# Optimization experiments

Measured on AMD Instinct MI355X. Metric: run time of the kernel, lower is better.

Reference implementation:

```python
import jax, jax.numpy as jnp
import numpy as np


def setup_inputs() -> dict:
    key = jax.random.key(0)
    kq, kk, kv, kl = jax.random.split(key, 4)
    B, Nq, Nk, D, Dv = 16, 2048, 2048, 128, 128
    queries = jax.random.normal(kq, (B, Nq, D), dtype=jnp.float32)
    keys = jax.random.normal(kk, (B, Nk, D), dtype=jnp.float32)
    values = jax.random.normal(kv, (B, Nk, Dv), dtype=jnp.float32)
    valid_lens = jax.random.randint(kl, (B,), 0, 2048, dtype=jnp.int64)
    return {"queries": queries, "keys": keys, "values": values, "valid_lens": valid_lens}


def reference(queries, keys, values, valid_lens):
    # queries: (B, Nq, d), keys: (B, Nk, d), values: (B, Nk, dv), valid_lens: (B,)
    d = queries.shape[-1]
    scores = jnp.einsum('bqd,bkd->bqk', queries, keys) / jnp.sqrt(jnp.asarray(d, queries.dtype))
    # masked_softmax: original sets masked score positions to 1e-8 (NOT -inf) before softmax
    nk = scores.shape[-1]
    mask = jnp.arange(nk)[None, :] < valid_lens[:, None]  # (B, Nk)
    scores = jnp.where(mask[:, None, :], scores, jnp.asarray(1e-8, scores.dtype))
    attn = jax.nn.softmax(scores, axis=-1)
    # dropout rate 0.0 -> identity (eval semantics)
    return jnp.einsum('bqk,bkv->bqv', attn, values)
```

## Files before the change

kernel.cpp:

```cpp
#include <hip/hip_runtime.h>
#include <stdint.h>

#define BATCH 16
#define NQ    2048
#define NK    2048
#define DD    128
#define DVV   128

typedef __bf16 bf16_t;
typedef __bf16 bf16x2 __attribute__((ext_vector_type(2)));
typedef __bf16 bf16x4 __attribute__((ext_vector_type(4)));
typedef __bf16 bf16x8 __attribute__((ext_vector_type(8)));
typedef float  f32x4  __attribute__((ext_vector_type(4)));

#define QB_OFF   ((size_t)0)
#define KB_OFF   ((size_t)8 * 1024 * 1024)
#define VT_OFF   ((size_t)16 * 1024 * 1024)
#define SUF_OFF  ((size_t)24 * 1024 * 1024)
#define SCH_OFF  (SUF_OFF + 65536)
#define WS_NEED  (SCH_OFF + 4096)

__device__ __forceinline__ int load_valid_len(const int* VL, int b) {
  bool looks64 = true;
#pragma unroll
  for (int i = 0; i < 16; ++i) {
    int hi = VL[2 * i + 1];
    unsigned lo = (unsigned)VL[2 * i];
    looks64 = looks64 && (hi == 0) && (lo <= 2048u);
  }
  int L = looks64 ? VL[2 * b] : VL[b];
  return min(max(L, 0), NK);
}

__device__ __forceinline__ void gld16(const void* g, void* l) {
  __builtin_amdgcn_global_load_lds(
      (const __attribute__((address_space(1))) unsigned int*)g,
      (__attribute__((address_space(3))) unsigned int*)l, 16, 0, 0);
}

__device__ __forceinline__ f32x4 mfma16(bf16x8 a, bf16x8 b, f32x4 c) {
  return __builtin_amdgcn_mfma_f32_16x16x32_bf16(a, b, c, 0, 0, 0);
}

__global__ void prep_kernel(const float* __restrict__ Q, const float* __restrict__ K,
                            const float* __restrict__ V, const int* __restrict__ VL,
                            bf16_t* __restrict__ Qb, bf16_t* __restrict__ Kb,
                            bf16_t* __restrict__ Vt, float* __restrict__ sufV,
                            int* __restrict__ sched) {
  __shared__ bf16_t tile[128 * 72];
  __shared__ int bs[16];
  const int bid = blockIdx.x;
  const int t = threadIdx.x;
  if (bid < 1024) {
    const float sc = 0.1275174307f;
    size_t base = ((size_t)bid * 256 + t) * 32;
    const size_t NQK = (size_t)BATCH * NQ * DD;
    bool isQ = base < NQK;
    const float* src = isQ ? (Q + base) : (K + (base - NQK));
    bf16_t* dst = isQ ? (Qb + base) : (Kb + (base - NQK));
    float s = isQ ? sc : 1.0f;
#pragma unroll
    for (int i = 0; i < 4; ++i) {
      float4 a = ((const float4*)src)[i * 2];
      float4 b = ((const float4*)src)[i * 2 + 1];
      bf16x8 o;
      o[0] = (bf16_t)(a.x * s); o[1] = (bf16_t)(a.y * s);
      o[2] = (bf16_t)(a.z * s); o[3] = (bf16_t)(a.w * s);
      o[4] = (bf16_t)(b.x * s); o[5] = (bf16_t)(b.y * s);
      o[6] = (bf16_t)(b.z * s); o[7] = (bf16_t)(b.w * s);
      ((bf16x8*)dst)[i] = o;
    }
    return;
  }
  if (bid < 1536) {
    int v = bid - 1024;
    int b = v & 15, kt = v >> 4;
    int L = load_valid_len(VL, b);
    int m = t & 31;
    int g = t >> 5;
    int r2 = m * 2;
    int k0g = kt * 64 + r2;
    const float* src = V + ((size_t)b * NK + k0g) * DVV;
    float sacc[4][4];
#pragma unroll
    for (int i = 0; i < 4; ++i)
#pragma unroll
      for (int j = 0; j < 4; ++j) sacc[i][j] = 0.f;
    bool a0 = (k0g >= L), a1 = (k0g + 1 >= L);
#pragma unroll
    for (int i = 0; i < 4; ++i) {
      int d4 = g * 4 + i * 32;
      float4 u0 = *(const float4*)(src + d4);
      float4 u1 = *(const float4*)(src + DVV + d4);
      *(bf16x2*)&tile[(d4 + 0) * 72 + r2] = (bf16x2){(bf16_t)u0.x, (bf16_t)u1.x};
      *(bf16x2*)&tile[(d4 + 1) * 72 + r2] = (bf16x2){(bf16_t)u0.y, (bf16_t)u1.y};
      *(bf16x2*)&tile[(d4 + 2) * 72 + r2] = (bf16x2){(bf16_t)u0.z, (bf16_t)u1.z};
      *(bf16x2*)&tile[(d4 + 3) * 72 + r2] = (bf16x2){(bf16_t)u0.w, (bf16_t)u1.w};
      if (a0) { sacc[i][0] += u0.x; sacc[i][1] += u0.y; sacc[i][2] += u0.z; sacc[i][3] += u0.w; }
      if (a1) { sacc[i][0] += u1.x; sacc[i][1] += u1.y; sacc[i][2] += u1.z; sacc[i][3] += u1.w; }
    }
    __syncthreads();
#pragma unroll
    for (int off = 1; off < 32; off <<= 1)
#pragma unroll
      for (int i = 0; i < 4; ++i)
#pragma unroll
        for (int j = 0; j < 4; ++j) sacc[i][j] += __shfl_xor(sacc[i][j], off, 64);
    if (m == 0) {
#pragma unroll
      for (int i = 0; i < 4; ++i)
#pragma unroll
        for (int j = 0; j < 4; ++j)
          atomicAdd(&sufV[b * 128 + g * 4 + i * 32 + j], sacc[i][j]);
    }
    int dv = t >> 1, half = t & 1;
    bf16_t* dst = Vt + (size_t)b * DVV * NK + (size_t)dv * NK + kt * 64 + half * 32;
    const bf16_t* srow = &tile[dv * 72 + half * 32];
#pragma unroll
    for (int j = 0; j < 4; ++j)
      *(bf16x8*)(dst + j * 8) = *(const bf16x8*)(srow + j * 8);
    return;
  }
  if (t == 0) {
    int Ls[16], idx[16];
#pragma unroll
    for (int i = 0; i < 16; ++i) { Ls[i] = load_valid_len(VL, i); idx[i] = i; }
    for (int i = 1; i < 16; ++i) {
      int lv = Ls[i], iv = idx[i], j = i - 1;
      while (j >= 0 && Ls[j] < lv) { Ls[j + 1] = Ls[j]; idx[j + 1] = idx[j]; --j; }
      Ls[j + 1] = lv; idx[j + 1] = iv;
    }
#pragma unroll
    for (int i = 0; i < 16; ++i) bs[i] = idx[i];
  }
  __syncthreads();
  for (int j = t; j < 512; j += 256) {
    int r = (j < 256) ? j : (767 - j);
    sched[j] = (bs[r >> 5] << 5) | (r & 31);
  }
}

__launch_bounds__(256, 2)
__global__ void attn_kernel(const bf16_t* __restrict__ Qb, const bf16_t* __restrict__ Kb,
                            const bf16_t* __restrict__ Vt, const int* __restrict__ VL,
                            const float* __restrict__ sufV, const int* __restrict__ sched,
                            float* __restrict__ Out) {
  __shared__ bf16_t sK[2][64 * 128];
  __shared__ bf16_t sVt[2][128 * 64];
  __shared__ bf16_t sP[4][16 * 64];

  const int unit = sched[blockIdx.x];
  const int b  = (unit >> 5) & 15;
  const int qt = unit & 31;
  const int L  = load_valid_len(VL, b);
  const int ktiles = (L + 63) >> 6;

  const int tid = threadIdx.x;
  const int wave = tid >> 6;
  const int lane = tid & 63;
  const int col = lane & 15;
  const int quad = lane >> 4;

  bf16x8 qf[4];
  {
    const bf16_t* qrow = Qb + ((size_t)b * NQ + qt * 64 + wave * 16 + col) * DD + quad * 8;
#pragma unroll
    for (int ks = 0; ks < 4; ++ks) qf[ks] = *(const bf16x8*)(qrow + ks * 32);
  }

  const char* Kbyte = (const char*)Kb + (size_t)b * NK * DD * 2;
  const char* Vbyte = (const char*)Vt + (size_t)b * DVV * NK * 2;
  int koff[4], voff[4];
#pragma unroll
  for (int i = 0; i < 4; ++i) {
    int krow = wave * 16 + i * 4 + (lane >> 4);
    koff[i] = krow * 256 + (((lane & 15) ^ (krow & 15)) * 16);
    int vrow = wave * 32 + i * 8 + (lane >> 3);
    voff[i] = vrow * (NK * 2) + (((lane & 7) ^ ((lane >> 3) & 7)) * 16);
  }
  bf16_t* pw = sP[wave];

  f32x4 Oacc[8];
#pragma unroll
  for (int o = 0; o < 8; ++o) Oacc[o] = (f32x4){0.f, 0.f, 0.f, 0.f};
  float lsum[4] = {0.f, 0.f, 0.f, 0.f};

  auto issueTile = [&](int kt, int bufi) {
    const char* kb = Kbyte + (size_t)kt * 16384;
    const char* vb = Vbyte + (size_t)kt * 128;
    bf16_t* kl = &sK[bufi][wave * 2048];
    bf16_t* vl = &sVt[bufi][wave * 2048];
#pragma unroll
    for (int i = 0; i < 4; ++i) {
      gld16(kb + koff[i], kl + i * 512);
      gld16(vb + voff[i], vl + i * 512);
    }
  };

  if (ktiles > 0) issueTile(0, 0);
  int bufi = 0;
  for (int kt = 0; kt < ktiles; ++kt) {
    if (kt + 1 < ktiles) {
      issueTile(kt + 1, bufi ^ 1);
      asm volatile("s_waitcnt vmcnt(8)\n\ts_barrier" ::: "memory");
    } else {
      asm volatile("s_waitcnt vmcnt(0)\n\ts_barrier" ::: "memory");
    }

    const bf16_t* kb_ = sK[bufi];
    const bf16_t* vb_ = sVt[bufi];

    f32x4 sc[4];
#pragma unroll
    for (int nt = 0; nt < 4; ++nt) sc[nt] = (f32x4){0.f, 0.f, 0.f, 0.f};
#pragma unroll
    for (int ks = 0; ks < 4; ++ks) {
      bf16x8 a = qf[ks];
#pragma unroll
      for (int nt = 0; nt < 4; ++nt) {
        bf16x8 bb = *(const bf16x8*)&kb_[(nt * 16 + col) * 128 + (((ks * 4 + quad) ^ col) * 8)];
        sc[nt] = mfma16(a, bb, sc[nt]);
      }
    }

    const int key0 = kt * 64;
#pragma unroll
    for (int nt = 0; nt < 4; ++nt) {
      bool valid = (key0 + nt * 16 + col) < L;
#pragma unroll
      for (int r = 0; r < 4; ++r) {
        float p = __builtin_amdgcn_exp2f(sc[nt][r]);
        p = valid ? p : 0.f;
        lsum[r] += p;
        int row = quad * 4 + r;
        int keyc = nt * 16 + col;
        int phys = ((keyc >> 3) ^ (row & 7));
        pw[row * 64 + phys * 8 + (keyc & 7)] = (bf16_t)p;
      }
    }

#pragma unroll
    for (int ks2 = 0; ks2 < 2; ++ks2) {
      bf16x8 a = *(const bf16x8*)&pw[col * 64 + (((ks2 * 4 + quad) ^ (col & 7)) * 8)];
#pragma unroll
      for (int o = 0; o < 8; ++o) {
        bf16x8 bb = *(const bf16x8*)&vb_[(o * 16 + col) * 64 + (((ks2 * 4 + quad) ^ (col & 7)) * 8)];
        Oacc[o] = mfma16(a, bb, Oacc[o]);
      }
    }
    asm volatile("s_barrier" ::: "memory");
    bufi ^= 1;
  }

#pragma unroll
  for (int off = 1; off < 16; off <<= 1)
#pragma unroll
    for (int r = 0; r < 4; ++r) lsum[r] += __shfl_xor(lsum[r], off, 64);

  const float wmask = (float)(NK - L);
  float invl[4];
#pragma unroll
  for (int r = 0; r < 4; ++r) invl[r] = 1.0f / (lsum[r] + wmask);
  const float* sfv = sufV + b * DVV;
  float* Ob = Out + ((size_t)b * NQ + qt * 64 + wave * 16) * DVV;
#pragma unroll
  for (int o = 0; o < 8; ++o) {
    float svv = sfv[o * 16 + col];
#pragma unroll
    for (int r = 0; r < 4; ++r)
      Ob[(size_t)(quad * 4 + r) * DVV + o * 16 + col] = (Oacc[o][r] + svv) * invl[r];
  }
}

#define KSTR 152
#define VSTR 88
#define PSTR 72

__global__ void suffix_fb(const float* __restrict__ V, const int* __restrict__ VL,
                          float* __restrict__ ws) {
  int b = blockIdx.x;
  int kc = blockIdx.y;
  int L = load_valid_len(VL, b);
  int k0 = kc * 128, k1 = k0 + 128;
  int lo = max(L, k0);
  int t = threadIdx.x;
  int dv = t & 127;
  int h = t >> 7;
  float s = 0.f;
  for (int k = lo + h; k < k1; k += 2)
    s += V[((size_t)b * NK + k) * DVV + dv];
  __shared__ float part[128];
  if (h == 0) part[dv] = s;
  __syncthreads();
  if (h == 1) atomicAdd(&ws[b * DVV + dv], part[dv] + s);
}

__launch_bounds__(256, 2)
__global__ void attn_fb(const float* __restrict__ Q, const float* __restrict__ K,
                        const float* __restrict__ V, const int* __restrict__ VL,
                        const float* __restrict__ sufV, float* __restrict__ Out) {
  const int flat = blockIdx.x;
  const int b  = flat & 15;
  const int qt = flat >> 4;
  const int L  = load_valid_len(VL, b);

  __shared__ bf16_t sK2[64 * KSTR];
  __shared__ bf16_t sVT2[128 * VSTR];
  __shared__ bf16_t sP2[4 * 16 * PSTR];

  const int tid  = threadIdx.x;
  const int wave = tid >> 6;
  const int lane = tid & 63;
  const int col  = lane & 15;
  const int quad = lane >> 4;

  const float* Qb = Q + ((size_t)b * NQ + qt * 64 + wave * 16) * DD;
  const float* Kb = K + (size_t)b * NK * DD;
  const float* Vb = V + (size_t)b * NK * DVV;

  bf16x8 qf[4];
  {
    const float scq = 0.08838834764831845f;
    const float* qrow = Qb + (size_t)col * DD + quad * 8;
#pragma unroll
    for (int ks = 0; ks < 4; ++ks) {
      float4 u0 = *(const float4*)(qrow + ks * 32);
      float4 u1 = *(const float4*)(qrow + ks * 32 + 4);
      bf16x8 f;
      f[0] = (bf16_t)(u0.x * scq); f[1] = (bf16_t)(u0.y * scq);
      f[2] = (bf16_t)(u0.z * scq); f[3] = (bf16_t)(u0.w * scq);
      f[4] = (bf16_t)(u1.x * scq); f[5] = (bf16_t)(u1.y * scq);
      f[6] = (bf16_t)(u1.z * scq); f[7] = (bf16_t)(u1.w * scq);
      qf[ks] = f;
    }
  }

  f32x4 Oacc[8];
#pragma unroll
  for (int o = 0; o < 8; ++o) Oacc[o] = (f32x4){0.f, 0.f, 0.f, 0.f};
  float m_i[4], l_i[4];
#pragma unroll
  for (int r = 0; r < 4; ++r) { m_i[r] = -1e30f; l_i[r] = 0.f; }

  const int ktiles = (L + 63) >> 6;
  for (int kt = 0; kt < ktiles; ++kt) {
    {
      int r0 = tid >> 5;
      int d4 = (tid & 31) * 4;
      const float* src = Kb + ((size_t)(kt * 64) + r0) * DD + d4;
#pragma unroll
      for (int i = 0; i < 8; ++i) {
        float4 u = *(const float4*)(src + (size_t)i * 8 * DD);
        bf16x4 w4 = {(bf16_t)u.x, (bf16_t)u.y, (bf16_t)u.z, (bf16_t)u.w};
        *(bf16x4*)&sK2[(r0 + i * 8) * KSTR + d4] = w4;
      }
    }
    {
      int r2 = (tid & 31) * 2;
      int dbase = (tid >> 5) * 4;
#pragma unroll
      for (int i = 0; i < 4; ++i) {
        int d4 = dbase + i * 32;
        const float* s0 = Vb + ((size_t)(kt * 64) + r2) * DVV + d4;
        float4 u0 = *(const float4*)s0;
        float4 u1 = *(const float4*)(s0 + DVV);
        *(bf16x2*)&sVT2[(d4 + 0) * VSTR + r2] = (bf16x2){(bf16_t)u0.x, (bf16_t)u1.x};
        *(bf16x2*)&sVT2[(d4 + 1) * VSTR + r2] = (bf16x2){(bf16_t)u0.y, (bf16_t)u1.y};
        *(bf16x2*)&sVT2[(d4 + 2) * VSTR + r2] = (bf16x2){(bf16_t)u0.z, (bf16_t)u1.z};
        *(bf16x2*)&sVT2[(d4 + 3) * VSTR + r2] = (bf16x2){(bf16_t)u0.w, (bf16_t)u1.w};
      }
    }
    __syncthreads();

    f32x4 sv4[4];
#pragma unroll
    for (int nt = 0; nt < 4; ++nt) sv4[nt] = (f32x4){0.f, 0.f, 0.f, 0.f};
#pragma unroll
    for (int ks = 0; ks < 4; ++ks) {
      bf16x8 a = qf[ks];
#pragma unroll
      for (int nt = 0; nt < 4; ++nt) {
        bf16x8 bb = *(const bf16x8*)&sK2[(nt * 16 + col) * KSTR + ks * 32 + quad * 8];
        sv4[nt] = mfma16(a, bb, sv4[nt]);
      }
    }

    const int key0 = kt * 64;
    float sv[4][4];
    float mloc[4] = {-1e30f, -1e30f, -1e30f, -1e30f};
#pragma unroll
    for (int nt = 0; nt < 4; ++nt) {
      int key = key0 + nt * 16 + col;
      bool valid = key < L;
#pragma unroll
      for (int r = 0; r < 4; ++r) {
        float v = valid ? sv4[nt][r] : -1e30f;
        sv[nt][r] = v;
        mloc[r] = fmaxf(mloc[r], v);
      }
    }
#pragma unroll
    for (int off = 1; off < 16; off <<= 1)
#pragma unroll
      for (int r = 0; r < 4; ++r) mloc[r] = fmaxf(mloc[r], __shfl_xor(mloc[r], off, 64));
    float al[4];
#pragma unroll
    for (int r = 0; r < 4; ++r) {
      float mn = fmaxf(m_i[r], mloc[r]);
      al[r] = __expf(m_i[r] - mn);
      m_i[r] = mn;
    }
    float lloc[4] = {0.f, 0.f, 0.f, 0.f};
#pragma unroll
    for (int nt = 0; nt < 4; ++nt)
#pragma unroll
      for (int r = 0; r < 4; ++r) {
        float p = __expf(sv[nt][r] - m_i[r]);
        sv[nt][r] = p;
        lloc[r] += p;
      }
#pragma unroll
    for (int off = 1; off < 16; off <<= 1)
#pragma unroll
      for (int r = 0; r < 4; ++r) lloc[r] += __shfl_xor(lloc[r], off, 64);
#pragma unroll
    for (int r = 0; r < 4; ++r) l_i[r] = l_i[r] * al[r] + lloc[r];
#pragma unroll
    for (int o = 0; o < 8; ++o)
#pragma unroll
      for (int r = 0; r < 4; ++r) Oacc[o][r] *= al[r];

    bf16_t* pw = &sP2[wave * 16 * PSTR];
#pragma unroll
    for (int nt = 0; nt < 4; ++nt)
#pragma unroll
      for (int r = 0; r < 4; ++r)
        pw[(quad * 4 + r) * PSTR + nt * 16 + col] = (bf16_t)sv[nt][r];

#pragma unroll
    for (int ks2 = 0; ks2 < 2; ++ks2) {
      bf16x8 a = *(const bf16x8*)&pw[(lane & 15) * PSTR + ks2 * 32 + quad * 8];
#pragma unroll
      for (int o = 0; o < 8; ++o) {
        bf16x8 bb = *(const bf16x8*)&sVT2[(o * 16 + col) * VSTR + ks2 * 32 + quad * 8];
        Oacc[o] = mfma16(a, bb, Oacc[o]);
      }
    }
    __syncthreads();
  }

  if (L < NK) {
    const float c = 1e-8f;
    const float w = (float)(NK - L);
    float a2[4], ec[4];
#pragma unroll
    for (int r = 0; r < 4; ++r) {
      float mn = fmaxf(m_i[r], c);
      a2[r] = __expf(m_i[r] - mn);
      ec[r] = __expf(c - mn);
      l_i[r] = l_i[r] * a2[r] + w * ec[r];
    }
    const float* sfv = sufV + b * DVV;
#pragma unroll
    for (int o = 0; o < 8; ++o) {
      float svv = sfv[o * 16 + col];
#pragma unroll
      for (int r = 0; r < 4; ++r) Oacc[o][r] = Oacc[o][r] * a2[r] + ec[r] * svv;
    }
  }

  float invl[4];
#pragma unroll
  for (int r = 0; r < 4; ++r) invl[r] = 1.0f / l_i[r];

  float* Ob = Out + ((size_t)b * NQ + qt * 64 + wave * 16) * DVV;
#pragma unroll
  for (int o = 0; o < 8; ++o)
#pragma unroll
    for (int r = 0; r < 4; ++r)
      Ob[(size_t)(quad * 4 + r) * DVV + o * 16 + col] = Oacc[o][r] * invl[r];
}

extern "C" void kernel_launch(void* const* d_in, const int* in_sizes, int n_in,
                              void* d_out, int out_size, void* d_ws, size_t ws_size,
                              hipStream_t stream) {
  const float* Q  = (const float*)d_in[0];
  const float* K  = (const float*)d_in[1];
  const float* V  = (const float*)d_in[2];
  const int*   VL = (const int*)d_in[3];
  float* out = (float*)d_out;

  if (ws_size >= WS_NEED) {
    char* ws = (char*)d_ws;
    bf16_t* Qb = (bf16_t*)(ws + QB_OFF);
    bf16_t* Kb = (bf16_t*)(ws + KB_OFF);
    bf16_t* Vt = (bf16_t*)(ws + VT_OFF);
    float* sufV = (float*)(ws + SUF_OFF);
    int* sched = (int*)(ws + SCH_OFF);

    hipMemsetAsync(sufV, 0, BATCH * DVV * sizeof(float), stream);
    prep_kernel<<<1537, 256, 0, stream>>>(Q, K, V, VL, Qb, Kb, Vt, sufV, sched);
    attn_kernel<<<512, 256, 0, stream>>>(Qb, Kb, Vt, VL, sufV, sched, out);
  } else {
    float* ws = (float*)d_ws;
    hipMemsetAsync(ws, 0, BATCH * DVV * sizeof(float), stream);
    dim3 g1(BATCH, 16);
    suffix_fb<<<g1, 256, 0, stream>>>(V, VL, ws);
    attn_fb<<<BATCH * (NQ / 64), 256, 0, stream>>>(Q, K, V, VL, ws, out);
  }
}
```

Baseline: 147.9 us.

## Split attention waves 2x2 over query rows and key columns with cross-wave reduction

Reorganizes attn_kernel so each wave handles 32 query rows and half of each 64-key tile (2x2 wave grid) instead of 16 rows over all keys. Each K and V fragment read from LDS now feeds two MFMAs, which halves LDS read traffic per MFMA. The cost is a partial O and rowsum reduction through shared memory at the end, plus more accumulator registers. The prep kernel's Q/K conversion also changes its indexing so consecutive threads access contiguous float4 pairs, for coalesced loads.

```diff
diff --git a/kernel.cpp b/kernel.cpp
--- a/kernel.cpp
+++ b/kernel.cpp
@@ -52,23 +52,23 @@
   const int bid = blockIdx.x;
   const int t = threadIdx.x;
   if (bid < 1024) {
-    const float sc = 0.1275174307f;
-    size_t base = ((size_t)bid * 256 + t) * 32;
-    const size_t NQK = (size_t)BATCH * NQ * DD;
-    bool isQ = base < NQK;
-    const float* src = isQ ? (Q + base) : (K + (base - NQK));
-    bf16_t* dst = isQ ? (Qb + base) : (Kb + (base - NQK));
-    float s = isQ ? sc : 1.0f;
+    const float scq = 0.1275174307f;
+    const size_t NQ4 = (size_t)BATCH * NQ * DD / 4;
 #pragma unroll
     for (int i = 0; i < 4; ++i) {
-      float4 a = ((const float4*)src)[i * 2];
-      float4 b = ((const float4*)src)[i * 2 + 1];
+      size_t idx = (size_t)bid * 2048 + (size_t)i * 512 + 2 * t;
+      bool isQ = idx < NQ4;
+      const float4* s4 = isQ ? ((const float4*)Q + idx) : ((const float4*)K + (idx - NQ4));
+      bf16x8* d8 = isQ ? ((bf16x8*)Qb + (idx >> 1)) : ((bf16x8*)Kb + ((idx - NQ4) >> 1));
+      float s = isQ ? scq : 1.0f;
+      float4 a = s4[0];
+      float4 b2 = s4[1];
       bf16x8 o;
       o[0] = (bf16_t)(a.x * s); o[1] = (bf16_t)(a.y * s);
       o[2] = (bf16_t)(a.z * s); o[3] = (bf16_t)(a.w * s);
-      o[4] = (bf16_t)(b.x * s); o[5] = (bf16_t)(b.y * s);
-      o[6] = (bf16_t)(b.z * s); o[7] = (bf16_t)(b.w * s);
-      ((bf16x8*)dst)[i] = o;
+      o[4] = (bf16_t)(b2.x * s); o[5] = (bf16_t)(b2.y * s);
+      o[6] = (bf16_t)(b2.z * s); o[7] = (bf16_t)(b2.w * s);
+      *d8 = o;
     }
     return;
   }
@@ -145,9 +145,9 @@
                             const bf16_t* __restrict__ Vt, const int* __restrict__ VL,
                             const float* __restrict__ sufV, const int* __restrict__ sched,
                             float* __restrict__ Out) {
-  __shared__ bf16_t sK[2][64 * 128];
-  __shared__ bf16_t sVt[2][128 * 64];
-  __shared__ bf16_t sP[4][16 * 64];
+  __shared__ __align__(16) char smem[73728];
+  bf16_t* sK = (bf16_t*)smem;
+  bf16_t* sV = (bf16_t*)(smem + 32768);
 
   const int unit = sched[blockIdx.x];
   const int b  = (unit >> 5) & 15;
@@ -160,12 +160,17 @@
   const int lane = tid & 63;
   const int col = lane & 15;
   const int quad = lane >> 4;
-
-  bf16x8 qf[4];
-  {
-    const bf16_t* qrow = Qb + ((size_t)b * NQ + qt * 64 + wave * 16 + col) * DD + quad * 8;
-#pragma unroll
-    for (int ks = 0; ks < 4; ++ks) qf[ks] = *(const bf16x8*)(qrow + ks * 32);
+  const int wr = wave >> 1;
+  const int wc = wave & 1;
+
+  bf16_t* pw = (bf16_t*)(smem + 65536 + wave * 2048);
+
+  bf16x8 qf[2][4];
+#pragma unroll
+  for (int m = 0; m < 2; ++m) {
+    const bf16_t* qrow = Qb + ((size_t)b * NQ + qt * 64 + wr * 32 + m * 16 + col) * DD + quad * 8;
+#pragma unroll
+    for (int ks = 0; ks < 4; ++ks) qf[m][ks] = *(const bf16x8*)(qrow + ks * 32);
   }
 
   const char* Kbyte = (const char*)Kb + (size_t)b * NK * DD * 2;
@@ -178,18 +183,23 @@
     int vrow = wave * 32 + i * 8 + (lane >> 3);
     voff[i] = vrow * (NK * 2) + (((lane & 7) ^ ((lane >> 3) & 7)) * 16);
   }
-  bf16_t* pw = sP[wave];
-
-  f32x4 Oacc[8];
-#pragma unroll
-  for (int o = 0; o < 8; ++o) Oacc[o] = (f32x4){0.f, 0.f, 0.f, 0.f};
-  float lsum[4] = {0.f, 0.f, 0.f, 0.f};
+
+  f32x4 Oacc[2][8];
+#pragma unroll
+  for (int m = 0; m < 2; ++m)
+#pragma unroll
+    for (int o = 0; o < 8; ++o) Oacc[m][o] = (f32x4){0.f, 0.f, 0.f, 0.f};
+  float lsum[2][4];
+#pragma unroll
+  for (int m = 0; m < 2; ++m)
+#pragma unroll
+    for (int r = 0; r < 4; ++r) lsum[m][r] = 0.f;
 
   auto issueTile = [&](int kt, int bufi) {
     const char* kb = Kbyte + (size_t)kt * 16384;
     const char* vb = Vbyte + (size_t)kt * 128;
-    bf16_t* kl = &sK[bufi][wave * 2048];
-    bf16_t* vl = &sVt[bufi][wave * 2048];
+    bf16_t* kl = sK + bufi * 8192 + wave * 2048;
+    bf16_t* vl = sV + bufi * 8192 + wave * 2048;
 #pragma unroll
     for (int i = 0; i < 4; ++i) {
       gld16(kb + koff[i], kl + i * 512);
@@ -207,46 +217,51 @@
       asm volatile("s_waitcnt vmcnt(0)\n\ts_barrier" ::: "memory");
     }
 
-    const bf16_t* kb_ = sK[bufi];
-    const bf16_t* vb_ = sVt[bufi];
-
-    f32x4 sc[4];
-#pragma unroll
-    for (int nt = 0; nt < 4; ++nt) sc[nt] = (f32x4){0.f, 0.f, 0.f, 0.f};
+    const bf16_t* kb_ = sK + bufi * 8192;
+    const bf16_t* vb_ = sV + bufi * 8192;
+
+    f32x4 sc[2][2];
+#pragma unroll
+    for (int m = 0; m < 2; ++m)
+#pragma unroll
+      for (int nt = 0; nt < 2; ++nt) sc[m][nt] = (f32x4){0.f, 0.f, 0.f, 0.f};
 #pragma unroll
     for (int ks = 0; ks < 4; ++ks) {
-      bf16x8 a = qf[ks];
-#pragma unroll
-      for (int nt = 0; nt < 4; ++nt) {
-        bf16x8 bb = *(const bf16x8*)&kb_[(nt * 16 + col) * 128 + (((ks * 4 + quad) ^ col) * 8)];
-        sc[nt] = mfma16(a, bb, sc[nt]);
-      }
-    }
-
-    const int key0 = kt * 64;
-#pragma unroll
-    for (int nt = 0; nt < 4; ++nt) {
+#pragma unroll
+      for (int nt = 0; nt < 2; ++nt) {
+        bf16x8 bb = *(const bf16x8*)&kb_[(wc * 32 + nt * 16 + col) * 128 + (((ks * 4 + quad) ^ col) * 8)];
+        sc[0][nt] = mfma16(qf[0][ks], bb, sc[0][nt]);
+        sc[1][nt] = mfma16(qf[1][ks], bb, sc[1][nt]);
+      }
+    }
+
+    const int key0 = kt * 64 + wc * 32;
+#pragma unroll
+    for (int nt = 0; nt < 2; ++nt) {
       bool valid = (key0 + nt * 16 + col) < L;
 #pragma unroll
-      for (int r = 0; r < 4; ++r) {
-        float p = __builtin_amdgcn_exp2f(sc[nt][r]);
-        p = valid ? p : 0.f;
-        lsum[r] += p;
-        int row = quad * 4 + r;
-        int keyc = nt * 16 + col;
-        int phys = ((keyc >> 3) ^ (row & 7));
-        pw[row * 64 + phys * 8 + (keyc & 7)] = (bf16_t)p;
-      }
-    }
-
-#pragma unroll
-    for (int ks2 = 0; ks2 < 2; ++ks2) {
-      bf16x8 a = *(const bf16x8*)&pw[col * 64 + (((ks2 * 4 + quad) ^ (col & 7)) * 8)];
-#pragma unroll
-      for (int o = 0; o < 8; ++o) {
-        bf16x8 bb = *(const bf16x8*)&vb_[(o * 16 + col) * 64 + (((ks2 * 4 + quad) ^ (col & 7)) * 8)];
-        Oacc[o] = mfma16(a, bb, Oacc[o]);
-      }
+      for (int m = 0; m < 2; ++m)
+#pragma unroll
+        for (int r = 0; r < 4; ++r) {
+          float p = __builtin_amdgcn_exp2f(sc[m][nt][r]);
+          p = valid ? p : 0.f;
+          lsum[m][r] += p;
+          int prow = quad * 4 + r;
+          int cidx = m * 4 + nt * 2 + (col >> 3);
+          int phys = cidx ^ (prow & 7);
+          pw[prow * 64 + phys * 8 + (col & 7)] = (bf16_t)p;
+        }
+    }
+
+    bf16x8 pa[2];
+#pragma unroll
+    for (int m = 0; m < 2; ++m)
+      pa[m] = *(const bf16x8*)&pw[col * 64 + (((m * 4 + quad) ^ (col & 7)) * 8)];
+#pragma unroll
+    for (int o = 0; o < 8; ++o) {
+      bf16x8 bb = *(const bf16x8*)&vb_[(o * 16 + col) * 64 + (((wc * 4 + quad) ^ (col & 7)) * 8)];
+      Oacc[0][o] = mfma16(pa[0], bb, Oacc[0][o]);
+      Oacc[1][o] = mfma16(pa[1], bb, Oacc[1][o]);
     }
     asm volatile("s_barrier" ::: "memory");
     bufi ^= 1;
@@ -255,20 +270,48 @@
 #pragma unroll
   for (int off = 1; off < 16; off <<= 1)
 #pragma unroll
-    for (int r = 0; r < 4; ++r) lsum[r] += __shfl_xor(lsum[r], off, 64);
-
-  const float wmask = (float)(NK - L);
-  float invl[4];
-#pragma unroll
-  for (int r = 0; r < 4; ++r) invl[r] = 1.0f / (lsum[r] + wmask);
-  const float* sfv = sufV + b * DVV;
-  float* Ob = Out + ((size_t)b * NQ + qt * 64 + wave * 16) * DVV;
-#pragma unroll
-  for (int o = 0; o < 8; ++o) {
-    float svv = sfv[o * 16 + col];
-#pragma unroll
-    for (int r = 0; r < 4; ++r)
-      Ob[(size_t)(quad * 4 + r) * DVV + o * 16 + col] = (Oacc[o][r] + svv) * invl[r];
+    for (int m = 0; m < 2; ++m)
+#pragma unroll
+      for (int r = 0; r < 4; ++r) lsum[m][r] += __shfl_xor(lsum[m][r], off, 64);
+
+  float* scrO = (float*)(smem + wr * 18432);
+  float* scrL = (float*)(smem + 65536) + wr * 32;
+
+  if (wc == 1) {
+#pragma unroll
+    for (int m = 0; m < 2; ++m)
+#pragma unroll
+      for (int o = 0; o < 8; ++o)
+        *(f32x4*)&scrO[(o * 16 + col) * 36 + m * 16 + quad * 4] = Oacc[m][o];
+    if (col == 0) {
+#pragma unroll
+      for (int m = 0; m < 2; ++m)
+#pragma unroll
+        for (int r = 0; r < 4; ++r) scrL[m * 16 + quad * 4 + r] = lsum[m][r];
+    }
+  }
+  __syncthreads();
+  if (wc == 0) {
+    const float wmask = (float)(NK - L);
+    float invl[2][4];
+#pragma unroll
+    for (int m = 0; m < 2; ++m)
+#pragma unroll
+      for (int r = 0; r < 4; ++r)
+        invl[m][r] = 1.0f / (lsum[m][r] + scrL[m * 16 + quad * 4 + r] + wmask);
+    const float* sfv = sufV + b * DVV;
+    float* Ob = Out + ((size_t)b * NQ + qt * 64 + wr * 32) * DVV;
+#pragma unroll
+    for (int m = 0; m < 2; ++m)
+#pragma unroll
+      for (int o = 0; o < 8; ++o) {
+        f32x4 part = *(const f32x4*)&scrO[(o * 16 + col) * 36 + m * 16 + quad * 4];
+        float svv = sfv[o * 16 + col];
+#pragma unroll
+        for (int r = 0; r < 4; ++r)
+          Ob[(size_t)(m * 16 + quad * 4 + r) * DVV + o * 16 + col] =
+              (Oacc[m][o][r] + part[r] + svv) * invl[m][r];
+      }
   }
 }
 
```

Measured after the change: 138.6 us. -6.3%, faster.
